# Optimization experiments

Hardware: AMD Instinct MI355X
Metric: run time of the kernel (lower is better)

Reference implementation:

```python
import jax, jax.numpy as jnp
import numpy as np

DECAY = 0.99


def setup_inputs() -> dict:
    key = jax.random.key(0)
    k1, k2, k3 = jax.random.split(key, 3)
    B, D, H, W = 16, 128, 32, 32
    K = 8192
    z_e = jax.random.normal(k1, (B, D, H, W), dtype=jnp.float32)
    codebook = jax.random.normal(k2, (K, D), dtype=jnp.float32)
    ema_count = jnp.ones((K,), dtype=jnp.float32)
    ema_weight = codebook  # buffer initialized as codebook.clone()
    return {"z_e": z_e, "codebook": codebook, "ema_count": ema_count, "ema_weight": ema_weight}


def reference(z_e, codebook, ema_count, ema_weight):
    B, D, H, W = z_e.shape
    K = codebook.shape[0]
    # (B,D,H,W) -> (N,D)
    z_flat = z_e.transpose(0, 2, 3, 1).reshape(-1, D)
    # squared L2 distances: ||z||^2 - 2 z.C^T + ||C||^2  -> (N,K)
    dist = (
        jnp.sum(z_flat * z_flat, axis=1, keepdims=True)
        - 2.0 * (z_flat @ codebook.T)
        + jnp.sum(codebook * codebook, axis=1)[None, :]
    )
    indices = jnp.argmin(dist, axis=1)  # (N,)
    z_q = codebook[indices].reshape(B, H, W, D).transpose(0, 3, 1, 2)
    # EMA codebook update (training path, no grad)
    counts = jax.ops.segment_sum(jnp.ones_like(indices, dtype=jnp.float32), indices, num_segments=K)
    dw = jax.ops.segment_sum(z_flat, indices, num_segments=K)  # (K,D)
    new_count = ema_count * DECAY + (1.0 - DECAY) * counts
    new_weight = ema_weight * DECAY + (1.0 - DECAY) * dw
    new_codebook = new_weight / jnp.maximum(new_count, 1.0)[:, None]
    # straight-through estimator
    z_q_st = z_e + jax.lax.stop_gradient(z_q - z_e)
    return (z_q_st, indices.reshape(B, H, W), new_codebook, new_count, new_weight)
```

## Files before the change

### kernel.cpp

```cpp
#include <hip/hip_runtime.h>

#define D 128
#define HW 1024
#define NROWS 16384
#define K 8192

#define OUT0 0
#define OUT1 2097152
#define OUT2 2113536
#define OUT3 3162112
#define OUT4 3170304

typedef __attribute__((ext_vector_type(8))) _Float16 half8;
typedef __attribute__((ext_vector_type(16))) float f32x16;
typedef unsigned short u16;
typedef unsigned long long u64;

__device__ __forceinline__ void gld16(const u16* gsrc, u16* ldst) {
    __builtin_amdgcn_global_load_lds(
        (const __attribute__((address_space(1))) unsigned int*)gsrc,
        (__attribute__((address_space(3))) unsigned int*)ldst,
        16, 0, 0);
}

__global__ __launch_bounds__(256) void k_prep_cb(const float* __restrict__ cb,
                                                 u16* __restrict__ Bg,
                                                 float* __restrict__ cnorm,
                                                 u64* __restrict__ packed,
                                                 float* __restrict__ counts,
                                                 float* __restrict__ dw) {
    const int tid = threadIdx.x;
    int kk = tid & 15;
    int k = blockIdx.x * 16 + (tid >> 4);
    const float* src = cb + (size_t)k * D + kk * 8;
    half8 h, l;
    float s = 0.f;
#pragma unroll
    for (int j = 0; j < 8; ++j) {
        float v = src[j];
        s += v * v;
        _Float16 hv = (_Float16)v;
        _Float16 lv = (_Float16)(v - (float)hv);
        h[j] = hv;
        l[j] = lv;
    }
    int g = k >> 6, col = k & 63, khalf = kk >> 3, kq = kk & 7;
    size_t base = ((size_t)(g * 2 + khalf)) * 8192 + ((size_t)kq * 64 + col) * 8;
    *(half8*)((_Float16*)Bg + base) = h;
    *(half8*)((_Float16*)Bg + base + 4096) = l;
#pragma unroll
    for (int off = 8; off > 0; off >>= 1) s += __shfl_down(s, off);
    if (kk == 0) cnorm[k] = s;
    float4 z4 = {0.f, 0.f, 0.f, 0.f};
    size_t zi = ((size_t)blockIdx.x * 256 + tid) * 8;
    *(float4*)(dw + zi) = z4;
    *(float4*)(dw + zi + 4) = z4;
    if (blockIdx.x < 64) packed[blockIdx.x * 256 + tid] = ~0ull;
    else if (blockIdx.x < 96) counts[(blockIdx.x - 64) * 256 + tid] = 0.f;
}

__global__ __launch_bounds__(256, 4) void k_argmin_mfma(
        const float* __restrict__ z_e,
        const u16* __restrict__ Bg,
        const float* __restrict__ cnorm, u64* __restrict__ packed) {
    __shared__ u16 lds[2][8192];

    const int tid = threadIdx.x;
    const int ln  = tid & 63;
    const int l31 = ln & 31;
    const int lh  = ln >> 5;
    const int wy  = (tid >> 6) & 1;
    const int wx  = tid >> 7;

    const int rg = blockIdx.x >> 2;
    const int k0 = (blockIdx.x & 3) * 2048;
    const int s0 = (k0 >> 6) * 2;

    const int rowA = rg * 64 + wy * 32 + l31;
    const float* za = z_e + (size_t)(rowA >> 10) * (D * HW) + (rowA & 1023);
    half8 Ah[8], Al[8];
#pragma unroll
    for (int ks = 0; ks < 8; ++ks) {
        half8 h, l;
#pragma unroll
        for (int j = 0; j < 8; ++j) {
            float v = za[(size_t)(ks * 16 + lh * 8 + j) * HW];
            _Float16 hv = (_Float16)v;
            _Float16 lv = (_Float16)(v - (float)hv);
            h[j] = hv;
            l[j] = lv;
        }
        Ah[ks] = h;
        Al[ks] = l;
    }

    {
        const u16* src = Bg + (size_t)s0 * 8192;
#pragma unroll
        for (int r = 0; r < 4; ++r)
            gld16(src + (r * 256 + tid) * 8, lds[0] + (r * 256 + tid) * 8);
    }

    float minv[16];
    int   mini[16];
#pragma unroll
    for (int r = 0; r < 16; ++r) { minv[r] = INFINITY; mini[r] = 0; }

    const int bo_base = wx * 32 + l31;

#pragma unroll 1
    for (int g = 0; g < 32; ++g) {
        const int colv = k0 + g * 64 + wx * 32 + l31;
        float cn0 = cnorm[colv];
        f32x16 acc = {};
#pragma unroll
        for (int half = 0; half < 2; ++half) {
            const int u = g * 2 + half;
            if (u + 1 < 64) {
                const u16* src = Bg + (size_t)(s0 + u + 1) * 8192;
                u16* dst = lds[1 - half];
#pragma unroll
                for (int r = 0; r < 4; ++r)
                    gld16(src + (r * 256 + tid) * 8, dst + (r * 256 + tid) * 8);
                asm volatile("s_waitcnt vmcnt(4)" ::: "memory");
            } else {
                asm volatile("s_waitcnt vmcnt(0)" ::: "memory");
            }
            asm volatile("s_barrier" ::: "memory");

            const _Float16* bh = (const _Float16*)lds[half];
#pragma unroll
            for (int ks = 0; ks < 4; ++ks) {
                const int bo = ((ks * 2 + lh) * 64 + bo_base) * 8;
                half8 bl = *(const half8*)(bh + 4096 + bo);
                half8 b0 = *(const half8*)(bh + bo);
                const int ak = half * 4 + ks;
                acc = __builtin_amdgcn_mfma_f32_32x32x16_f16(Ah[ak], bl, acc, 0, 0, 0);
                acc = __builtin_amdgcn_mfma_f32_32x32x16_f16(Ah[ak], b0, acc, 0, 0, 0);
                acc = __builtin_amdgcn_mfma_f32_32x32x16_f16(Al[ak], b0, acc, 0, 0, 0);
            }
            asm volatile("s_barrier" ::: "memory");
        }
#pragma unroll
        for (int r = 0; r < 16; ++r) {
            float d0 = fmaf(-2.0f, acc[r], cn0);
            if (d0 < minv[r]) { minv[r] = d0; mini[r] = colv; }
        }
    }

#pragma unroll
    for (int r = 0; r < 16; ++r) {
        float v = minv[r];
        int ix = mini[r];
#pragma unroll
        for (int off = 1; off < 32; off <<= 1) {
            float v2 = __shfl_xor(v, off);
            int i2 = __shfl_xor(ix, off);
            if (v2 < v || (v2 == v && i2 < ix)) { v = v2; ix = i2; }
        }
        if (l31 == 0) {
            int row = rg * 64 + wy * 32 + 4 * lh + (r & 3) + 8 * (r >> 2);
            unsigned int uenc = __float_as_uint(v);
            uenc = (uenc & 0x80000000u) ? ~uenc : (uenc | 0x80000000u);
            u64 pk = ((u64)uenc << 13) | (u64)(unsigned)ix;
            atomicMin(&packed[row], pk);
        }
    }
}

__global__ __launch_bounds__(256) void k_epilogue(const float* __restrict__ z_e,
                                                  const float* __restrict__ cb,
                                                  const u64* __restrict__ packed,
                                                  float* __restrict__ out0,
                                                  float* __restrict__ out1,
                                                  float* __restrict__ counts,
                                                  float* __restrict__ dw) {
    __shared__ int idxS[64];
    const int tid = threadIdx.x;
    const int n0 = blockIdx.x * 64;
    const int bb = n0 >> 10, p0 = n0 & 1023;

    if (tid < 64) {
        int ix = (int)(packed[n0 + tid] & 0x1FFFull);
        idxS[tid] = ix;
        out1[n0 + tid] = (float)ix;
        atomicAdd(&counts[ix], 1.0f);
    }
    __syncthreads();

    const float* zb = z_e + (size_t)bb * (D * HW) + p0;
    float* ob = out0 + (size_t)bb * (D * HW) + p0;

    for (int i = tid; i < 64 * D; i += 256) {
        int d = i >> 6, r = i & 63;
        float z = zb[(size_t)d * HW + r];
        float c = cb[(size_t)idxS[r] * D + d];
        ob[(size_t)d * HW + r] = z + (c - z);
    }
    for (int i = tid; i < 64 * D; i += 256) {
        int r = i >> 7, d = i & 127;
        atomicAdd(&dw[(size_t)idxS[r] * D + d], zb[(size_t)d * HW + r]);
    }
}

__global__ __launch_bounds__(256) void k_final(const float* __restrict__ ema_count,
                                               const float* __restrict__ ema_weight,
                                               float* __restrict__ out2,
                                               float* __restrict__ out3,
                                               float* __restrict__ out4) {
    int gid = blockIdx.x * 256 + threadIdx.x;
    int k = gid >> 7, d = gid & 127;
    float cnt_raw = out3[k];
    float dw_raw = out4[gid];
    __syncthreads();
    float nc = 0.99f * ema_count[k] + 0.01f * cnt_raw;
    float nw = 0.99f * ema_weight[gid] + 0.01f * dw_raw;
    out4[gid] = nw;
    out2[gid] = nw / fmaxf(nc, 1.0f);
    if (d == 0) out3[k] = nc;
}

extern "C" void kernel_launch(void* const* d_in, const int* in_sizes, int n_in,
                              void* d_out, int out_size, void* d_ws, size_t ws_size,
                              hipStream_t stream) {
    const float* z_e        = (const float*)d_in[0];
    const float* cb         = (const float*)d_in[1];
    const float* ema_count  = (const float*)d_in[2];
    const float* ema_weight = (const float*)d_in[3];
    float* out = (float*)d_out;

    float* cnorm = (float*)d_ws;
    u64* packed = (u64*)((char*)d_ws + K * 4);

    u16* Bg = (u16*)(out + OUT2);

    k_prep_cb    <<<K / 16,        256, 0, stream>>>(cb, Bg, cnorm, packed,
                                                     out + OUT3, out + OUT4);
    k_argmin_mfma<<<1024,          256, 0, stream>>>(z_e, Bg, cnorm, packed);
    k_epilogue   <<<NROWS / 64,    256, 0, stream>>>(z_e, cb, packed,
                                                     out + OUT0, out + OUT1,
                                                     out + OUT3, out + OUT4);
    k_final      <<<(K * D) / 256, 256, 0, stream>>>(ema_count, ema_weight,
                                                     out + OUT2, out + OUT3, out + OUT4);
}
```

Before: 227.2 us.

## Double row tile per wave in argmin kernel to reuse codebook LDS fragments

Each wave now computes two 32-row tiles against each codebook chunk, so every B fragment read from LDS feeds two MFMA chains, and each block covers 128 rows instead of 64, halving the grid. The codebook staging layout is regrouped so a full 64-column, 128-depth chunk (hi and lo halves) is loaded per stage, which halves the number of barrier pairs per block. The goal is less codebook reload traffic and LDS bandwidth per MFMA. The cost is double the register footprint for A fragments, accumulators and running minima, with occupancy bounds lowered from 4 to 2 and LDS doubled, which may limit latency hiding. Only 512 blocks remain, so the device is also less fully occupied.

```diff
diff --git a/kernel.cpp b/kernel.cpp
--- a/kernel.cpp
+++ b/kernel.cpp
@@ -4,6 +4,7 @@
 #define HW 1024
 #define NROWS 16384
 #define K 8192
+#define NU 32
 
 #define OUT0 0
 #define OUT1 2097152
@@ -44,10 +45,10 @@
         h[j] = hv;
         l[j] = lv;
     }
-    int g = k >> 6, col = k & 63, khalf = kk >> 3, kq = kk & 7;
-    size_t base = ((size_t)(g * 2 + khalf)) * 8192 + ((size_t)kq * 64 + col) * 8;
-    *(half8*)((_Float16*)Bg + base) = h;
-    *(half8*)((_Float16*)Bg + base + 4096) = l;
+    int g = k >> 6, col = k & 63;
+    size_t offH = (size_t)g * 16384 + ((size_t)kk * 64 + col) * 8;
+    *(half8*)((_Float16*)Bg + offH) = h;
+    *(half8*)((_Float16*)Bg + offH + 8192) = l;
 #pragma unroll
     for (int off = 8; off > 0; off >>= 1) s += __shfl_down(s, off);
     if (kk == 0) cnorm[k] = s;
@@ -59,11 +60,11 @@
     else if (blockIdx.x < 96) counts[(blockIdx.x - 64) * 256 + tid] = 0.f;
 }
 
-__global__ __launch_bounds__(256, 4) void k_argmin_mfma(
+__global__ __launch_bounds__(256, 2) void k_argmin_mfma(
         const float* __restrict__ z_e,
         const u16* __restrict__ Bg,
         const float* __restrict__ cnorm, u64* __restrict__ packed) {
-    __shared__ u16 lds[2][8192];
+    __shared__ u16 lds[2][16384];
 
     const int tid = threadIdx.x;
     const int ln  = tid & 63;
@@ -74,98 +75,108 @@
 
     const int rg = blockIdx.x >> 2;
     const int k0 = (blockIdx.x & 3) * 2048;
-    const int s0 = (k0 >> 6) * 2;
-
-    const int rowA = rg * 64 + wy * 32 + l31;
-    const float* za = z_e + (size_t)(rowA >> 10) * (D * HW) + (rowA & 1023);
-    half8 Ah[8], Al[8];
-#pragma unroll
-    for (int ks = 0; ks < 8; ++ks) {
-        half8 h, l;
-#pragma unroll
-        for (int j = 0; j < 8; ++j) {
-            float v = za[(size_t)(ks * 16 + lh * 8 + j) * HW];
-            _Float16 hv = (_Float16)v;
-            _Float16 lv = (_Float16)(v - (float)hv);
-            h[j] = hv;
-            l[j] = lv;
-        }
-        Ah[ks] = h;
-        Al[ks] = l;
+    const int g0 = k0 >> 6;
+
+    half8 Ah[2][8], Al[2][8];
+#pragma unroll
+    for (int rt = 0; rt < 2; ++rt) {
+        const int rowA = rg * 128 + wy * 64 + rt * 32 + l31;
+        const float* za = z_e + (size_t)(rowA >> 10) * (D * HW) + (rowA & 1023);
+#pragma unroll
+        for (int ks = 0; ks < 8; ++ks) {
+            half8 h, l;
+#pragma unroll
+            for (int j = 0; j < 8; ++j) {
+                float v = za[(size_t)(ks * 16 + lh * 8 + j) * HW];
+                _Float16 hv = (_Float16)v;
+                _Float16 lv = (_Float16)(v - (float)hv);
+                h[j] = hv;
+                l[j] = lv;
+            }
+            Ah[rt][ks] = h;
+            Al[rt][ks] = l;
+        }
     }
 
     {
-        const u16* src = Bg + (size_t)s0 * 8192;
-#pragma unroll
-        for (int r = 0; r < 4; ++r)
+        const u16* src = Bg + (size_t)g0 * 16384;
+#pragma unroll
+        for (int r = 0; r < 8; ++r)
             gld16(src + (r * 256 + tid) * 8, lds[0] + (r * 256 + tid) * 8);
     }
 
-    float minv[16];
-    int   mini[16];
-#pragma unroll
-    for (int r = 0; r < 16; ++r) { minv[r] = INFINITY; mini[r] = 0; }
+    float minv[2][16];
+    int   mini[2][16];
+#pragma unroll
+    for (int rt = 0; rt < 2; ++rt)
+#pragma unroll
+        for (int r = 0; r < 16; ++r) { minv[rt][r] = INFINITY; mini[rt][r] = 0; }
 
     const int bo_base = wx * 32 + l31;
 
 #pragma unroll 1
-    for (int g = 0; g < 32; ++g) {
-        const int colv = k0 + g * 64 + wx * 32 + l31;
+    for (int u = 0; u < NU; ++u) {
+        const int colv = k0 + u * 64 + wx * 32 + l31;
         float cn0 = cnorm[colv];
-        f32x16 acc = {};
-#pragma unroll
-        for (int half = 0; half < 2; ++half) {
-            const int u = g * 2 + half;
-            if (u + 1 < 64) {
-                const u16* src = Bg + (size_t)(s0 + u + 1) * 8192;
-                u16* dst = lds[1 - half];
-#pragma unroll
-                for (int r = 0; r < 4; ++r)
-                    gld16(src + (r * 256 + tid) * 8, dst + (r * 256 + tid) * 8);
-                asm volatile("s_waitcnt vmcnt(4)" ::: "memory");
-            } else {
-                asm volatile("s_waitcnt vmcnt(0)" ::: "memory");
+
+        if (u + 1 < NU) {
+            const u16* src = Bg + (size_t)(g0 + u + 1) * 16384;
+            u16* dst = lds[(u + 1) & 1];
+#pragma unroll
+            for (int r = 0; r < 8; ++r)
+                gld16(src + (r * 256 + tid) * 8, dst + (r * 256 + tid) * 8);
+            asm volatile("s_waitcnt vmcnt(8)" ::: "memory");
+        } else {
+            asm volatile("s_waitcnt vmcnt(0)" ::: "memory");
+        }
+        asm volatile("s_barrier" ::: "memory");
+
+        const _Float16* bh = (const _Float16*)lds[u & 1];
+        const _Float16* bl = bh + 8192;
+        f32x16 acc0 = {}, acc1 = {};
+#pragma unroll
+        for (int ks = 0; ks < 8; ++ks) {
+            const int bo = ((ks * 2 + lh) * 64 + bo_base) * 8;
+            half8 vbl = *(const half8*)(bl + bo);
+            half8 vbh = *(const half8*)(bh + bo);
+            acc0 = __builtin_amdgcn_mfma_f32_32x32x16_f16(Ah[0][ks], vbl, acc0, 0, 0, 0);
+            acc1 = __builtin_amdgcn_mfma_f32_32x32x16_f16(Ah[1][ks], vbl, acc1, 0, 0, 0);
+            acc0 = __builtin_amdgcn_mfma_f32_32x32x16_f16(Ah[0][ks], vbh, acc0, 0, 0, 0);
+            acc1 = __builtin_amdgcn_mfma_f32_32x32x16_f16(Ah[1][ks], vbh, acc1, 0, 0, 0);
+            acc0 = __builtin_amdgcn_mfma_f32_32x32x16_f16(Al[0][ks], vbh, acc0, 0, 0, 0);
+            acc1 = __builtin_amdgcn_mfma_f32_32x32x16_f16(Al[1][ks], vbh, acc1, 0, 0, 0);
+        }
+
+#pragma unroll
+        for (int r = 0; r < 16; ++r) {
+            float d0 = fmaf(-2.0f, acc0[r], cn0);
+            float d1 = fmaf(-2.0f, acc1[r], cn0);
+            if (d0 < minv[0][r]) { minv[0][r] = d0; mini[0][r] = colv; }
+            if (d1 < minv[1][r]) { minv[1][r] = d1; mini[1][r] = colv; }
+        }
+        asm volatile("s_barrier" ::: "memory");
+    }
+
+#pragma unroll
+    for (int rt = 0; rt < 2; ++rt)
+#pragma unroll
+        for (int r = 0; r < 16; ++r) {
+            float v = minv[rt][r];
+            int ix = mini[rt][r];
+#pragma unroll
+            for (int off = 1; off < 32; off <<= 1) {
+                float v2 = __shfl_xor(v, off);
+                int i2 = __shfl_xor(ix, off);
+                if (v2 < v || (v2 == v && i2 < ix)) { v = v2; ix = i2; }
             }
-            asm volatile("s_barrier" ::: "memory");
-
-            const _Float16* bh = (const _Float16*)lds[half];
-#pragma unroll
-            for (int ks = 0; ks < 4; ++ks) {
-                const int bo = ((ks * 2 + lh) * 64 + bo_base) * 8;
-                half8 bl = *(const half8*)(bh + 4096 + bo);
-                half8 b0 = *(const half8*)(bh + bo);
-                const int ak = half * 4 + ks;
-                acc = __builtin_amdgcn_mfma_f32_32x32x16_f16(Ah[ak], bl, acc, 0, 0, 0);
-                acc = __builtin_amdgcn_mfma_f32_32x32x16_f16(Ah[ak], b0, acc, 0, 0, 0);
-                acc = __builtin_amdgcn_mfma_f32_32x32x16_f16(Al[ak], b0, acc, 0, 0, 0);
+            if (l31 == 0) {
+                int row = rg * 128 + wy * 64 + rt * 32 + 4 * lh + (r & 3) + 8 * (r >> 2);
+                unsigned int uenc = __float_as_uint(v);
+                uenc = (uenc & 0x80000000u) ? ~uenc : (uenc | 0x80000000u);
+                u64 pk = ((u64)uenc << 13) | (u64)(unsigned)ix;
+                atomicMin(&packed[row], pk);
             }
-            asm volatile("s_barrier" ::: "memory");
-        }
-#pragma unroll
-        for (int r = 0; r < 16; ++r) {
-            float d0 = fmaf(-2.0f, acc[r], cn0);
-            if (d0 < minv[r]) { minv[r] = d0; mini[r] = colv; }
-        }
-    }
-
-#pragma unroll
-    for (int r = 0; r < 16; ++r) {
-        float v = minv[r];
-        int ix = mini[r];
-#pragma unroll
-        for (int off = 1; off < 32; off <<= 1) {
-            float v2 = __shfl_xor(v, off);
-            int i2 = __shfl_xor(ix, off);
-            if (v2 < v || (v2 == v && i2 < ix)) { v = v2; ix = i2; }
-        }
-        if (l31 == 0) {
-            int row = rg * 64 + wy * 32 + 4 * lh + (r & 3) + 8 * (r >> 2);
-            unsigned int uenc = __float_as_uint(v);
-            uenc = (uenc & 0x80000000u) ? ~uenc : (uenc | 0x80000000u);
-            u64 pk = ((u64)uenc << 13) | (u64)(unsigned)ix;
-            atomicMin(&packed[row], pk);
-        }
-    }
+        }
 }
 
 __global__ __launch_bounds__(256) void k_epilogue(const float* __restrict__ z_e,
@@ -236,7 +247,7 @@
 
     k_prep_cb    <<<K / 16,        256, 0, stream>>>(cb, Bg, cnorm, packed,
                                                      out + OUT3, out + OUT4);
-    k_argmin_mfma<<<1024,          256, 0, stream>>>(z_e, Bg, cnorm, packed);
+    k_argmin_mfma<<<512,           256, 0, stream>>>(z_e, Bg, cnorm, packed);
     k_epilogue   <<<NROWS / 64,    256, 0, stream>>>(z_e, cb, packed,
                                                      out + OUT0, out + OUT1,
                                                      out + OUT3, out + OUT4);
```

Result: faster. 209.7 us (-7.7%).
